# Performance work log

Hardware: AMD Instinct MI355X
Metric: run time of the kernel (lower is better)

Reference implementation:

```python
import jax, jax.numpy as jnp
import numpy as np

NUM_HEADS = 16

def setup_inputs() -> dict:
    key = jax.random.key(0)
    k1, k2, k3 = jax.random.split(key, 3)
    B, S, D = 2, 2048, 1024
    return {
        "hidden_states": jax.random.normal(k1, (B, S, D), dtype=jnp.float32),
        "W_attn": jax.random.normal(k2, (D, 3 * D), dtype=jnp.float32) * 0.02,
        "b_attn": jnp.zeros((3 * D,), dtype=jnp.float32),
        "W_proj": jax.random.normal(k3, (D, D), dtype=jnp.float32) * 0.02,
        "b_proj": jnp.zeros((D,), dtype=jnp.float32),
    }

def reference(hidden_states, W_attn, b_attn, W_proj, b_proj):
    B, S, D = hidden_states.shape
    H = NUM_HEADS
    hd = D // H
    # qkv projection (Conv1D == addmm): [B,S,3D]
    qkv = hidden_states @ W_attn + b_attn
    q, k, v = jnp.split(qkv, 3, axis=-1)
    # split heads -> [B,H,S,hd]
    def split_heads(t):
        return t.reshape(B, S, H, hd).transpose(0, 2, 1, 3)
    q, k, v = split_heads(q), split_heads(k), split_heads(v)
    # scaled QK^T: [B,H,S,S]
    scores = jnp.einsum('bhqd,bhkd->bhqk', q, k) / jnp.asarray(hd ** 0.5, dtype=q.dtype)
    causal = jnp.tril(jnp.ones((S, S), dtype=bool))
    mask_value = jnp.finfo(scores.dtype).min
    scores = jnp.where(causal, scores, mask_value)
    probs = jax.nn.softmax(scores, axis=-1)  # attn_pdrop=0 -> no dropout
    out = jnp.einsum('bhqk,bhkd->bhqd', probs, v)
    # merge heads -> [B,S,D]
    out = out.transpose(0, 2, 1, 3).reshape(B, S, D)
    out = out @ W_proj + b_proj  # resid_pdrop=0 -> no dropout
    return out
```

## Files before the change

kernel.cpp:

```cpp
#include <hip/hip_runtime.h>
#include <math.h>

typedef __attribute__((ext_vector_type(8))) short bf16x8;
typedef __attribute__((ext_vector_type(4))) short bf16x4;
typedef __attribute__((ext_vector_type(4))) float f32x4;

#define MFMA16(a, b, c) __builtin_amdgcn_mfma_f32_16x16x32_bf16(a, b, c, 0, 0, 0)

#define GLOAD_LDS16(g, l)                                                        \
    __builtin_amdgcn_global_load_lds(                                            \
        (const __attribute__((address_space(1))) void*)(g),                      \
        (__attribute__((address_space(3))) void*)(l), 16, 0, 0)

__device__ __forceinline__ short f2bf(float f) {
    union { float f; unsigned u; } x; x.f = f;
    unsigned r = (x.u + 0x7fffu + ((x.u >> 16) & 1u)) >> 16;
    return (short)r;
}

__global__ __launch_bounds__(256) void convert_bf16_kernel(
    const float* __restrict__ in, short* __restrict__ out, int n4) {
    int i = blockIdx.x * 256 + threadIdx.x;
    if (i >= n4) return;
    float4 v = ((const float4*)in)[i];
    bf16x4 o;
    o[0] = f2bf(v.x); o[1] = f2bf(v.y); o[2] = f2bf(v.z); o[3] = f2bf(v.w);
    ((bf16x4*)out)[i] = o;
}

__global__ __launch_bounds__(256) void transpose_w2_kernel(
    const float* __restrict__ Wa, const float* __restrict__ Wp,
    short* __restrict__ WaT, short* __restrict__ WpT) {
    __shared__ float tile[32][33];
    const float* W; short* Wt; int N, xb;
    if (blockIdx.x < 96) { W = Wa; Wt = WaT; N = 3072; xb = blockIdx.x; }
    else                 { W = Wp; Wt = WpT; N = 1024; xb = blockIdx.x - 96; }
    const int K = 1024;
    int c = threadIdx.x & 31, r0 = threadIdx.x >> 5;
    int n0 = xb << 5, k0 = blockIdx.y << 5;
#pragma unroll
    for (int i = 0; i < 4; i++) {
        int r = r0 + i * 8;
        tile[r][c] = W[(long)(k0 + r) * N + n0 + c];
    }
    __syncthreads();
#pragma unroll
    for (int i = 0; i < 4; i++) {
        int r = r0 + i * 8;
        Wt[(long)(n0 + r) * K + k0 + c] = f2bf(tile[c][r]);
    }
}

template <int EPI>
__global__ __launch_bounds__(256) void gemm_bt_kernel(
    const short* __restrict__ A, const short* __restrict__ Bt,
    const float* __restrict__ bias, float* __restrict__ outF,
    short* __restrict__ qkv, short* __restrict__ VTb,
    int M, int N, int Kdim) {
    __shared__ __align__(16) short lsAll[17408];
    short* lsA = lsAll;
    short* lsB = lsAll + 8192;
    const int tid = threadIdx.x;
    const int lane = tid & 63, l15 = lane & 15, quad = lane >> 4;
    const int w = tid >> 6, wm = w >> 1, wn = w & 1;
    const int m0 = blockIdx.y * 128, n0 = blockIdx.x * 128;
    const int e = l15 & 7;
    const int lrow = lane >> 3;
    const int lgcol = ((lane & 7) ^ lrow) << 3;

    f32x4 acc[4][4];
#pragma unroll
    for (int i = 0; i < 4; i++)
#pragma unroll
        for (int j = 0; j < 4; j++) acc[i][j] = (f32x4){0.f, 0.f, 0.f, 0.f};

    for (int k0 = 0; k0 < Kdim; k0 += 64) {
#pragma unroll
        for (int ii = 0; ii < 4; ii++) {
            const int i = (w << 2) + ii;
            const int grow = (i << 3) + lrow;
            GLOAD_LDS16(&A[(size_t)(m0 + grow) * Kdim + k0 + lgcol], &lsA[i * 512]);
            GLOAD_LDS16(&Bt[(size_t)(n0 + grow) * Kdim + k0 + lgcol], &lsB[i * 512]);
        }
        __syncthreads();
#pragma unroll
        for (int kk = 0; kk < 64; kk += 32) {
            const int kb = kk >> 3;
            bf16x8 af[4], bfr[4];
#pragma unroll
            for (int t = 0; t < 4; t++) {
                const int sw = (((kb + quad) ^ e) << 3);
                af[t] = *(const bf16x8*)&lsA[(wm * 64 + t * 16 + l15) * 64 + sw];
                bfr[t] = *(const bf16x8*)&lsB[(wn * 64 + t * 16 + l15) * 64 + sw];
            }
#pragma unroll
            for (int mt = 0; mt < 4; mt++)
#pragma unroll
                for (int nt = 0; nt < 4; nt++)
                    acc[mt][nt] = MFMA16(af[mt], bfr[nt], acc[mt][nt]);
        }
        __syncthreads();
    }

    if (EPI == 0) {
#pragma unroll
        for (int nt = 0; nt < 4; nt++) {
            int nn = n0 + wn * 64 + nt * 16 + l15;
            float bv = bias[nn];
#pragma unroll
            for (int mt = 0; mt < 4; mt++)
#pragma unroll
                for (int r = 0; r < 4; r++) {
                    int mm = m0 + wm * 64 + mt * 16 + quad * 4 + r;
                    outF[(long)mm * N + nn] = acc[mt][nt][r] + bv;
                }
        }
    } else if (n0 < 2048) {
        const float scale = (n0 < 1024) ? 0.18033688011112042f : 1.0f;
#pragma unroll
        for (int nt = 0; nt < 4; nt++) {
            int nn = n0 + wn * 64 + nt * 16 + l15;
            float bv = bias[nn];
#pragma unroll
            for (int mt = 0; mt < 4; mt++)
#pragma unroll
                for (int r = 0; r < 4; r++) {
                    int mm = m0 + wm * 64 + mt * 16 + quad * 4 + r;
                    qkv[(long)mm * 3072 + nn] = f2bf((acc[mt][nt][r] + bv) * scale);
                }
        }
    } else {
        short* vt = &lsAll[w * (64 * 68)];
#pragma unroll
        for (int nt = 0; nt < 4; nt++) {
            int nn = n0 + wn * 64 + nt * 16 + l15;
            float bv = bias[nn];
#pragma unroll
            for (int mt = 0; mt < 4; mt++) {
                bf16x4 pk;
#pragma unroll
                for (int r = 0; r < 4; r++) pk[r] = f2bf(acc[mt][nt][r] + bv);
                *(bf16x4*)&vt[(nt * 16 + l15) * 68 + mt * 16 + quad * 4] = pk;
            }
        }
        const int hh = ((n0 - 2048) >> 6) + wn;
        const int bb = m0 >> 11;
        const int srow = (m0 & 2047) + wm * 64;
        const int sloc = (lane & 7) << 3;
#pragma unroll
        for (int i = 0; i < 8; i++) {
            const int d = i * 8 + (lane >> 3);
            bf16x8 vv = *(const bf16x8*)&vt[d * 68 + sloc];
            *(bf16x8*)&VTb[((size_t)(bb * 16 + hh) * 64 + d) * 2048 + srow + sloc] = vv;
        }
    }
}

__global__ __launch_bounds__(256, 4) void attn_kernel(
    const short* __restrict__ qkv, const short* __restrict__ VT,
    short* __restrict__ Ao) {
    __shared__ __align__(16) short Kt[2][64 * 64];
    __shared__ __align__(16) short Vt[2][64 * 64];
    __shared__ __align__(16) short Pt[4][1024];
    const int tid = threadIdx.x;
    const int lane = tid & 63, l15 = lane & 15, quad = lane >> 4, w = tid >> 6;
    const int bx = blockIdx.x;
    const int qt = 31 - (bx >> 5);
    const int hb = bx & 31;
    const int b = hb >> 4, h = hb & 15;
    const size_t rowbase = (size_t)b * 2048 * 3072 + h * 64;
    const short* Qb = qkv + rowbase;
    const short* Kb = qkv + rowbase + 1024;
    const short* Vh = VT + (size_t)hb * 64 * 2048;
    short* Pw = &Pt[w][0];
    const int e = l15 & 7;

    const int srow0 = tid >> 3, sc40 = (tid & 7) ^ (srow0 & 7);
    const int srow1 = srow0 + 32, sc41 = (tid & 7) ^ (srow1 & 7);
    const int sdst0 = srow0 * 64 + ((tid & 7) << 3);
    const int sdst1 = srow1 * 64 + ((tid & 7) << 3);

    const long qr = (long)(qt * 64 + w * 16 + l15) * 3072;
    bf16x8 qf0 = *(const bf16x8*)&Qb[qr + quad * 8];
    bf16x8 qf1 = *(const bf16x8*)&Qb[qr + 32 + quad * 8];

    float l = 0.f;
    f32x4 o[4];
#pragma unroll
    for (int dt = 0; dt < 4; dt++) o[dt] = (f32x4){0.f, 0.f, 0.f, 0.f};

    const int nc = qt + 1;

    *(bf16x8*)&Kt[0][sdst0] = *(const bf16x8*)&Kb[(size_t)srow0 * 3072 + sc40 * 8];
    *(bf16x8*)&Kt[0][sdst1] = *(const bf16x8*)&Kb[(size_t)srow1 * 3072 + sc41 * 8];
    *(bf16x8*)&Vt[0][sdst0] = *(const bf16x8*)&Vh[srow0 * 2048 + sc40 * 8];
    *(bf16x8*)&Vt[0][sdst1] = *(const bf16x8*)&Vh[srow1 * 2048 + sc41 * 8];
    __syncthreads();

    for (int c = 0; c < nc; c++) {
        const short* Kc = &Kt[c & 1][0];
        const short* Vc = &Vt[c & 1][0];
        const bool more = (c + 1 < nc);
        bf16x8 kr0, kr1, vr0, vr1;
        if (more) {
            const int k2 = (c + 1) * 64;
            kr0 = *(const bf16x8*)&Kb[(size_t)(k2 + srow0) * 3072 + sc40 * 8];
            kr1 = *(const bf16x8*)&Kb[(size_t)(k2 + srow1) * 3072 + sc41 * 8];
            vr0 = *(const bf16x8*)&Vh[srow0 * 2048 + k2 + sc40 * 8];
            vr1 = *(const bf16x8*)&Vh[srow1 * 2048 + k2 + sc41 * 8];
        }

        f32x4 s[4];
#pragma unroll
        for (int t = 0; t < 4; t++) {
            bf16x8 k0f = *(const bf16x8*)&Kc[(t * 16 + l15) * 64 + ((quad ^ e) << 3)];
            bf16x8 k1f = *(const bf16x8*)&Kc[(t * 16 + l15) * 64 + (((4 + quad) ^ e) << 3)];
            f32x4 z = (f32x4){0.f, 0.f, 0.f, 0.f};
            z = MFMA16(k0f, qf0, z);
            z = MFMA16(k1f, qf1, z);
            s[t] = z;
        }

        if (c == nc - 1) {
#pragma unroll
            for (int t = 0; t < 4; t++)
#pragma unroll
                for (int r = 0; r < 4; r++)
                    if (t * 16 + quad * 4 + r > w * 16 + l15) s[t][r] = -INFINITY;
        }

#pragma unroll
        for (int t = 0; t < 4; t++) {
            bf16x4 pw;
#pragma unroll
            for (int r = 0; r < 4; r++) {
                float pv = __builtin_amdgcn_exp2f(s[t][r]);
                l += pv;
                pw[r] = f2bf(pv);
            }
            *(bf16x4*)&Pw[l15 * 64 + (((2 * t + (quad >> 1)) ^ e) << 3) + ((quad & 1) << 2)] = pw;
        }

        bf16x8 pf0 = *(const bf16x8*)&Pw[l15 * 64 + ((quad ^ e) << 3)];
        bf16x8 pf1 = *(const bf16x8*)&Pw[l15 * 64 + (((4 + quad) ^ e) << 3)];
#pragma unroll
        for (int dt = 0; dt < 4; dt++) {
            bf16x8 v0f = *(const bf16x8*)&Vc[(dt * 16 + l15) * 64 + ((quad ^ e) << 3)];
            bf16x8 v1f = *(const bf16x8*)&Vc[(dt * 16 + l15) * 64 + (((4 + quad) ^ e) << 3)];
            o[dt] = MFMA16(v0f, pf0, o[dt]);
            o[dt] = MFMA16(v1f, pf1, o[dt]);
        }

        if (more) {
            short* Kn = &Kt[(c + 1) & 1][0];
            short* Vn = &Vt[(c + 1) & 1][0];
            *(bf16x8*)&Kn[sdst0] = kr0;
            *(bf16x8*)&Kn[sdst1] = kr1;
            *(bf16x8*)&Vn[sdst0] = vr0;
            *(bf16x8*)&Vn[sdst1] = vr1;
        }
        __syncthreads();
    }

    l += __shfl_xor(l, 16);
    l += __shfl_xor(l, 32);
    const float rl = 1.f / l;

    const int qs = qt * 64 + w * 16 + l15;
    const long base = ((long)(b * 2048 + qs)) * 1024 + h * 64;
#pragma unroll
    for (int dt = 0; dt < 4; dt++) {
        bf16x4 wv;
#pragma unroll
        for (int r = 0; r < 4; r++) wv[r] = f2bf(o[dt][r] * rl);
        *(bf16x4*)&Ao[base + dt * 16 + quad * 4] = wv;
    }
}

extern "C" void kernel_launch(void* const* d_in, const int* in_sizes, int n_in,
                              void* d_out, int out_size, void* d_ws, size_t ws_size,
                              hipStream_t stream) {
    const float* hs = (const float*)d_in[0];
    const float* W_attn = (const float*)d_in[1];
    const float* b_attn = (const float*)d_in[2];
    const float* W_proj = (const float*)d_in[3];
    const float* b_proj = (const float*)d_in[4];
    float* out = (float*)d_out;

    char* ws = (char*)d_ws;
    short* hs_bf = (short*)ws;
    short* attn_o = hs_bf;
    short* WaT = (short*)(ws + 8u * 1024 * 1024);
    short* WpT = (short*)(ws + 14u * 1024 * 1024);
    short* qkv = (short*)(ws + 16u * 1024 * 1024);
    short* VTb = (short*)(ws + 40u * 1024 * 1024);

    convert_bf16_kernel<<<4096, 256, 0, stream>>>(hs, hs_bf, 1048576);
    transpose_w2_kernel<<<dim3(128, 32), 256, 0, stream>>>(W_attn, W_proj, WaT, WpT);
    gemm_bt_kernel<1><<<dim3(24, 32), 256, 0, stream>>>(
        hs_bf, WaT, b_attn, nullptr, qkv, VTb, 4096, 3072, 1024);
    attn_kernel<<<1024, 256, 0, stream>>>(qkv, VTb, attn_o);
    gemm_bt_kernel<0><<<dim3(8, 32), 256, 0, stream>>>(
        attn_o, WpT, b_proj, out, nullptr, nullptr, 4096, 1024, 1024);
}
```

Baseline: 186.0 us.

## Use 32x32 MFMA and 128-row query tiles in causal attention kernel

The attention kernel now gives each workgroup 128 query rows (32 per wave) and runs QK^T and PV with 32x32x16 bf16 MFMAs instead of 16x16x32. Each K/V tile loaded into LDS is shared by twice as many queries, and the grid is halved. Waves whose query rows lie entirely before a key chunk skip its compute. The costs are more registers (launch bounds lowered to 3 blocks per CU), idle waves in the diagonal chunks, and fewer blocks to balance the triangular workload.

Measured after the change: 195.4 us. 5.0% more time.

```diff
diff --git a/kernel.cpp b/kernel.cpp
--- a/kernel.cpp
+++ b/kernel.cpp
@@ -4,8 +4,10 @@
 typedef __attribute__((ext_vector_type(8))) short bf16x8;
 typedef __attribute__((ext_vector_type(4))) short bf16x4;
 typedef __attribute__((ext_vector_type(4))) float f32x4;
+typedef __attribute__((ext_vector_type(16))) float f32x16;
 
 #define MFMA16(a, b, c) __builtin_amdgcn_mfma_f32_16x16x32_bf16(a, b, c, 0, 0, 0)
+#define MFMA32(a, b, c) __builtin_amdgcn_mfma_f32_32x32x16_bf16(a, b, c, 0, 0, 0)
 
 #define GLOAD_LDS16(g, l)                                                        \
     __builtin_amdgcn_global_load_lds(                                            \
@@ -16,6 +18,13 @@
     union { float f; unsigned u; } x; x.f = f;
     unsigned r = (x.u + 0x7fffu + ((x.u >> 16) & 1u)) >> 16;
     return (short)r;
+}
+
+__device__ __forceinline__ f32x16 zero16() {
+    f32x16 z;
+#pragma unroll
+    for (int i = 0; i < 16; i++) z[i] = 0.f;
+    return z;
 }
 
 __global__ __launch_bounds__(256) void convert_bf16_kernel(
@@ -156,16 +165,16 @@
     }
 }
 
-__global__ __launch_bounds__(256, 4) void attn_kernel(
+__global__ __launch_bounds__(256, 3) void attn_kernel(
     const short* __restrict__ qkv, const short* __restrict__ VT,
     short* __restrict__ Ao) {
     __shared__ __align__(16) short Kt[2][64 * 64];
     __shared__ __align__(16) short Vt[2][64 * 64];
-    __shared__ __align__(16) short Pt[4][1024];
+    __shared__ __align__(16) short Pt[4][32 * 64];
     const int tid = threadIdx.x;
-    const int lane = tid & 63, l15 = lane & 15, quad = lane >> 4, w = tid >> 6;
+    const int lane = tid & 63, col = lane & 31, hi = lane >> 5, w = tid >> 6;
     const int bx = blockIdx.x;
-    const int qt = 31 - (bx >> 5);
+    const int qt = 15 - (bx >> 5);
     const int hb = bx & 31;
     const int b = hb >> 4, h = hb & 15;
     const size_t rowbase = (size_t)b * 2048 * 3072 + h * 64;
@@ -173,23 +182,26 @@
     const short* Kb = qkv + rowbase + 1024;
     const short* Vh = VT + (size_t)hb * 64 * 2048;
     short* Pw = &Pt[w][0];
-    const int e = l15 & 7;
 
     const int srow0 = tid >> 3, sc40 = (tid & 7) ^ (srow0 & 7);
     const int srow1 = srow0 + 32, sc41 = (tid & 7) ^ (srow1 & 7);
     const int sdst0 = srow0 * 64 + ((tid & 7) << 3);
     const int sdst1 = srow1 * 64 + ((tid & 7) << 3);
 
-    const long qr = (long)(qt * 64 + w * 16 + l15) * 3072;
-    bf16x8 qf0 = *(const bf16x8*)&Qb[qr + quad * 8];
-    bf16x8 qf1 = *(const bf16x8*)&Qb[qr + 32 + quad * 8];
+    const int qloc = w * 32 + col;
+    const int qglob = qt * 128 + qloc;
+
+    bf16x8 qf[4];
+#pragma unroll
+    for (int kc = 0; kc < 4; kc++)
+        qf[kc] = *(const bf16x8*)&Qb[(long)qglob * 3072 + kc * 16 + hi * 8];
 
     float l = 0.f;
-    f32x4 o[4];
-#pragma unroll
-    for (int dt = 0; dt < 4; dt++) o[dt] = (f32x4){0.f, 0.f, 0.f, 0.f};
-
-    const int nc = qt + 1;
+    f32x16 o[2];
+    o[0] = zero16(); o[1] = zero16();
+
+    const int nc = 2 * qt + 2;
+    const int ca = 2 * qt + (w >> 1);
 
     *(bf16x8*)&Kt[0][sdst0] = *(const bf16x8*)&Kb[(size_t)srow0 * 3072 + sc40 * 8];
     *(bf16x8*)&Kt[0][sdst1] = *(const bf16x8*)&Kb[(size_t)srow1 * 3072 + sc41 * 8];
@@ -210,45 +222,63 @@
             vr1 = *(const bf16x8*)&Vh[srow1 * 2048 + k2 + sc41 * 8];
         }
 
-        f32x4 s[4];
-#pragma unroll
-        for (int t = 0; t < 4; t++) {
-            bf16x8 k0f = *(const bf16x8*)&Kc[(t * 16 + l15) * 64 + ((quad ^ e) << 3)];
-            bf16x8 k1f = *(const bf16x8*)&Kc[(t * 16 + l15) * 64 + (((4 + quad) ^ e) << 3)];
-            f32x4 z = (f32x4){0.f, 0.f, 0.f, 0.f};
-            z = MFMA16(k0f, qf0, z);
-            z = MFMA16(k1f, qf1, z);
-            s[t] = z;
-        }
-
-        if (c == nc - 1) {
-#pragma unroll
-            for (int t = 0; t < 4; t++)
-#pragma unroll
-                for (int r = 0; r < 4; r++)
-                    if (t * 16 + quad * 4 + r > w * 16 + l15) s[t][r] = -INFINITY;
-        }
-
-#pragma unroll
-        for (int t = 0; t < 4; t++) {
-            bf16x4 pw;
-#pragma unroll
-            for (int r = 0; r < 4; r++) {
-                float pv = __builtin_amdgcn_exp2f(s[t][r]);
-                l += pv;
-                pw[r] = f2bf(pv);
-            }
-            *(bf16x4*)&Pw[l15 * 64 + (((2 * t + (quad >> 1)) ^ e) << 3) + ((quad & 1) << 2)] = pw;
-        }
-
-        bf16x8 pf0 = *(const bf16x8*)&Pw[l15 * 64 + ((quad ^ e) << 3)];
-        bf16x8 pf1 = *(const bf16x8*)&Pw[l15 * 64 + (((4 + quad) ^ e) << 3)];
-#pragma unroll
-        for (int dt = 0; dt < 4; dt++) {
-            bf16x8 v0f = *(const bf16x8*)&Vc[(dt * 16 + l15) * 64 + ((quad ^ e) << 3)];
-            bf16x8 v1f = *(const bf16x8*)&Vc[(dt * 16 + l15) * 64 + (((4 + quad) ^ e) << 3)];
-            o[dt] = MFMA16(v0f, pf0, o[dt]);
-            o[dt] = MFMA16(v1f, pf1, o[dt]);
+        if (c <= ca) {
+            f32x16 s[2];
+#pragma unroll
+            for (int t = 0; t < 2; t++) {
+                f32x16 z = zero16();
+#pragma unroll
+                for (int kc = 0; kc < 4; kc++) {
+                    const int row = t * 32 + col;
+                    bf16x8 kf = *(const bf16x8*)&Kc[row * 64 + (((kc * 2 + hi) ^ (row & 7)) << 3)];
+                    z = MFMA32(kf, qf[kc], z);
+                }
+                s[t] = z;
+            }
+
+            if (c == ca) {
+#pragma unroll
+                for (int t = 0; t < 2; t++) {
+                    const int thresh = qloc + qt * 128 - c * 64 - t * 32;
+#pragma unroll
+                    for (int g = 0; g < 4; g++)
+#pragma unroll
+                        for (int r2 = 0; r2 < 4; r2++) {
+                            const int row = r2 + 8 * g + 4 * hi;
+                            if (row > thresh) s[t][g * 4 + r2] = -INFINITY;
+                        }
+                }
+            }
+
+#pragma unroll
+            for (int t = 0; t < 2; t++) {
+#pragma unroll
+                for (int g = 0; g < 4; g++) {
+                    bf16x4 pw;
+#pragma unroll
+                    for (int r2 = 0; r2 < 4; r2++) {
+                        float pv = __builtin_amdgcn_exp2f(s[t][g * 4 + r2]);
+                        l += pv;
+                        pw[r2] = f2bf(pv);
+                    }
+                    *(bf16x4*)&Pw[col * 64 + (((t * 4 + g) ^ (col & 7)) << 3) + hi * 4] = pw;
+                }
+            }
+
+            bf16x8 pf[4];
+#pragma unroll
+            for (int kc2 = 0; kc2 < 4; kc2++)
+                pf[kc2] = *(const bf16x8*)&Pw[col * 64 + (((kc2 * 2 + hi) ^ (col & 7)) << 3)];
+
+#pragma unroll
+            for (int dt = 0; dt < 2; dt++) {
+                const int vrow = dt * 32 + col;
+#pragma unroll
+                for (int kc2 = 0; kc2 < 4; kc2++) {
+                    bf16x8 vf = *(const bf16x8*)&Vc[vrow * 64 + (((kc2 * 2 + hi) ^ (vrow & 7)) << 3)];
+                    o[dt] = MFMA32(vf, pf[kc2], o[dt]);
+                }
+            }
         }
 
         if (more) {
@@ -262,18 +292,19 @@
         __syncthreads();
     }
 
-    l += __shfl_xor(l, 16);
     l += __shfl_xor(l, 32);
     const float rl = 1.f / l;
 
-    const int qs = qt * 64 + w * 16 + l15;
-    const long base = ((long)(b * 2048 + qs)) * 1024 + h * 64;
-#pragma unroll
-    for (int dt = 0; dt < 4; dt++) {
-        bf16x4 wv;
-#pragma unroll
-        for (int r = 0; r < 4; r++) wv[r] = f2bf(o[dt][r] * rl);
-        *(bf16x4*)&Ao[base + dt * 16 + quad * 4] = wv;
+    const long base = ((long)(b * 2048 + qglob)) * 1024 + h * 64;
+#pragma unroll
+    for (int dt = 0; dt < 2; dt++) {
+#pragma unroll
+        for (int g = 0; g < 4; g++) {
+            bf16x4 wv;
+#pragma unroll
+            for (int r2 = 0; r2 < 4; r2++) wv[r2] = f2bf(o[dt][g * 4 + r2] * rl);
+            *(bf16x4*)&Ao[base + dt * 32 + g * 8 + hi * 4] = wv;
+        }
     }
 }
 
@@ -299,7 +330,7 @@
     transpose_w2_kernel<<<dim3(128, 32), 256, 0, stream>>>(W_attn, W_proj, WaT, WpT);
     gemm_bt_kernel<1><<<dim3(24, 32), 256, 0, stream>>>(
         hs_bf, WaT, b_attn, nullptr, qkv, VTb, 4096, 3072, 1024);
-    attn_kernel<<<1024, 256, 0, stream>>>(qkv, VTb, attn_o);
+    attn_kernel<<<512, 256, 0, stream>>>(qkv, VTb, attn_o);
     gemm_bt_kernel<0><<<dim3(8, 32), 256, 0, stream>>>(
         attn_o, WpT, b_proj, out, nullptr, nullptr, 4096, 1024, 1024);
 }
```
